# Kernel tuning notes

Measured on AMD Instinct MI355X. Metric: run time of the kernel, lower is better.

## Reference

```python
import jax, jax.numpy as jnp
import numpy as np

B, E, D, H = 4096, 16, 512, 2048

def setup_inputs() -> dict:
    key = jax.random.key(0)
    k1, k2, k3, k4 = jax.random.split(key, 4)
    semantic_vec = jax.random.normal(k1, (B, D), dtype=jnp.float32)
    field_centers = jax.random.normal(k2, (E, D), dtype=jnp.float32)
    # Kaiming-uniform-ish Linear init scale
    lim = 1.0 / np.sqrt(D)
    W = jax.random.uniform(k3, (E, H, D), dtype=jnp.float32, minval=-lim, maxval=lim)
    b = jax.random.uniform(k4, (E, H), dtype=jnp.float32, minval=-lim, maxval=lim)
    return {"semantic_vec": semantic_vec, "field_centers": field_centers, "W": W, "b": b}

def reference(semantic_vec, field_centers, W, b):
    # Each expert e: relu((x - c_e) @ W_e^T + b_e); sum over experts.
    # Use linearity: (x - c_e) @ W_e^T = x @ W_e^T - c_e @ W_e^T, avoiding the [B,E,D] offsets tensor.
    xw = jnp.einsum('bd,ehd->beh', semantic_vec, W)          # [B,E,H]
    cw = jnp.einsum('ed,ehd->eh', field_centers, W)          # [E,H]
    pre = xw - cw[None, :, :] + b[None, :, :]                # [B,E,H]
    feature_anchor = jnp.sum(jax.nn.relu(pre), axis=1)       # [B,H]
    return feature_anchor
```

## Files before the change

### kernel.cpp

```cpp
#include <hip/hip_runtime.h>
#include <hip/hip_bf16.h>
#include <stdint.h>
#include <stddef.h>


#define B_DIM 4096
#define E_DIM 16
#define D_DIM 512
#define H_DIM 2048

typedef short bf16x8 __attribute__((ext_vector_type(8)));
typedef float f32x4 __attribute__((ext_vector_type(4)));

__device__ __forceinline__ short f2bf(float f) {
  __hip_bfloat16 h = __float2bfloat16(f);
  return *reinterpret_cast<short*>(&h);
}

__device__ __forceinline__ bf16x8 cvt8(float4 a, float4 b) {
  bf16x8 v;
  v[0] = f2bf(a.x); v[1] = f2bf(a.y); v[2] = f2bf(a.z); v[3] = f2bf(a.w);
  v[4] = f2bf(b.x); v[5] = f2bf(b.y); v[6] = f2bf(b.z); v[7] = f2bf(b.w);
  return v;
}

__device__ __forceinline__ void async_copy16(const void* gptr, void* lptr) {
  __builtin_amdgcn_global_load_lds(
      (const __attribute__((address_space(1))) void*)gptr,
      (__attribute__((address_space(3))) void*)lptr,
      16, 0, 0);
}

__global__ __launch_bounds__(256) void prep_w(
    const float* __restrict__ W, const float* __restrict__ C,
    const float* __restrict__ bias, __hip_bfloat16* __restrict__ Wb,
    float* __restrict__ bias2) {
  const int gw = (blockIdx.x * 256 + threadIdx.x) >> 6;
  const int lane = threadIdx.x & 63;
  const int e = gw >> 11;

  const float* wr = W + (size_t)gw * D_DIM + lane * 8;
  const float* cr = C + (size_t)e * D_DIM + lane * 8;
  float4 w0 = *(const float4*)(wr);
  float4 w1 = *(const float4*)(wr + 4);
  float4 c0 = *(const float4*)(cr);
  float4 c1 = *(const float4*)(cr + 4);

  *(bf16x8*)((__hip_bfloat16*)Wb + (size_t)gw * D_DIM + lane * 8) = cvt8(w0, w1);

  float dot = w0.x * c0.x + w0.y * c0.y + w0.z * c0.z + w0.w * c0.w +
              w1.x * c1.x + w1.y * c1.y + w1.z * c1.z + w1.w * c1.w;
#pragma unroll
  for (int off = 32; off > 0; off >>= 1) dot += __shfl_down(dot, off, 64);
  if (lane == 0) bias2[gw] = bias[gw] - dot;
}

__global__ __launch_bounds__(256) void conv_x(
    const float* __restrict__ X, __hip_bfloat16* __restrict__ Xb) {
  const size_t i = ((size_t)blockIdx.x * 256 + threadIdx.x) * 8;
  float4 a = *(const float4*)(X + i);
  float4 b = *(const float4*)(X + i + 4);
  *(bf16x8*)(Xb + i) = cvt8(a, b);
}

__global__ __launch_bounds__(256, 2) void moe_gemm(
    const __hip_bfloat16* __restrict__ Xb,
    const __hip_bfloat16* __restrict__ Wb,
    const float* __restrict__ bias2,
    float* __restrict__ out) {
  __shared__ __align__(16) __hip_bfloat16 As[2][128 * 32];
  __shared__ __align__(16) __hip_bfloat16 Bs0[2][128 * 32];
  __shared__ __align__(16) __hip_bfloat16 Bs1[2][128 * 32];
  __shared__ __align__(16) float biasS[E_DIM * 128];

  const int tid = threadIdx.x;
  const int lane = tid & 63;
  const int wave = tid >> 6;
  const int hi = blockIdx.x & 15;
  const int mi = blockIdx.x >> 4;
  const int m0 = mi * 128;
  const int h0 = hi * 128;

  for (int idx = tid; idx < E_DIM * 128; idx += 256) {
    biasS[idx] = bias2[((idx >> 7) << 7 << 4) + h0 + (idx & 127)];
  }

  const int wm = (wave & 1) * 64;
  const int wn = (wave >> 1) * 64;
  const int lm = lane & 15;
  const int q = lane >> 4;

  const int r = tid >> 2;
  const int col = (tid & 3) << 3;
  const size_t aOff0 = (size_t)(m0 + r) * D_DIM + col;
  const size_t aOff1 = (size_t)(m0 + r + 64) * D_DIM + col;
  const size_t bOff0 = (size_t)(h0 + r) * D_DIM + col;
  const size_t bOff1 = (size_t)(h0 + r + 64) * D_DIM + col;
  const int ld0 = tid * 8;
  const int ld1 = (tid + 256) * 8;

  int offA[4], offB[4];
#pragma unroll
  for (int i = 0; i < 4; ++i) offA[i] = (wm + i * 16 + lm) * 32 + q * 8;
#pragma unroll
  for (int j = 0; j < 4; ++j) offB[j] = (wn + j * 16 + lm) * 32 + q * 8;

  f32x4 sum[4][4], acc0[4][4], acc1[4][4];
#pragma unroll
  for (int i = 0; i < 4; ++i)
#pragma unroll
    for (int j = 0; j < 4; ++j) {
      sum[i][j] = (f32x4){0.f, 0.f, 0.f, 0.f};
      acc0[i][j] = (f32x4){0.f, 0.f, 0.f, 0.f};
      acc1[i][j] = (f32x4){0.f, 0.f, 0.f, 0.f};
    }

#define STAGE(buf, tt)                                                       \
  {                                                                          \
    const int kk = ((tt) & 15) << 5;                                         \
    const __hip_bfloat16* Bb = Wb + ((size_t)((tt) >> 4) << 21);             \
    async_copy16(Xb + aOff0 + kk, &As[buf][ld0]);                            \
    async_copy16(Xb + aOff1 + kk, &As[buf][ld1]);                            \
    async_copy16(Bb + bOff0 + kk, &Bs0[buf][ld0]);                           \
    async_copy16(Bb + bOff1 + kk, &Bs0[buf][ld1]);                           \
    async_copy16(Bb + bOff0 + kk + (size_t)H_DIM * D_DIM, &Bs1[buf][ld0]);   \
    async_copy16(Bb + bOff1 + kk + (size_t)H_DIM * D_DIM, &Bs1[buf][ld1]);   \
  }

  STAGE(0, 0);
  __syncthreads();

  for (int t = 0; t < 128; ++t) {
    const int cur = t & 1;
    if (t < 127) STAGE(cur ^ 1, t + 1);

    bf16x8 af[4];
#pragma unroll
    for (int i = 0; i < 4; ++i) af[i] = *(const bf16x8*)&As[cur][offA[i]];
#pragma unroll
    for (int j = 0; j < 4; ++j) {
      const bf16x8 b0 = *(const bf16x8*)&Bs0[cur][offB[j]];
#pragma unroll
      for (int i = 0; i < 4; ++i)
        acc0[i][j] = __builtin_amdgcn_mfma_f32_16x16x32_bf16(
            af[i], b0, acc0[i][j], 0, 0, 0);
      const bf16x8 b1 = *(const bf16x8*)&Bs1[cur][offB[j]];
#pragma unroll
      for (int i = 0; i < 4; ++i)
        acc1[i][j] = __builtin_amdgcn_mfma_f32_16x16x32_bf16(
            af[i], b1, acc1[i][j], 0, 0, 0);
    }

    if ((t & 15) == 15) {
      const int pair = t >> 4;
#pragma unroll
      for (int j = 0; j < 4; ++j) {
        const float bv0 = biasS[(2 * pair) * 128 + wn + j * 16 + lm];
        const float bv1 = biasS[(2 * pair + 1) * 128 + wn + j * 16 + lm];
#pragma unroll
        for (int i = 0; i < 4; ++i)
#pragma unroll
          for (int u = 0; u < 4; ++u) {
            sum[i][j][u] += fmaxf(acc0[i][j][u] + bv0, 0.f) +
                            fmaxf(acc1[i][j][u] + bv1, 0.f);
            acc0[i][j][u] = 0.f;
            acc1[i][j][u] = 0.f;
          }
      }
    }

    __syncthreads();
  }
#undef STAGE

  const int rbase = q * 4;
#pragma unroll
  for (int i = 0; i < 4; ++i)
#pragma unroll
    for (int j = 0; j < 4; ++j)
#pragma unroll
      for (int u = 0; u < 4; ++u)
        out[(size_t)(m0 + wm + i * 16 + rbase + u) * H_DIM + h0 + wn + j * 16 + lm] =
            sum[i][j][u];
}

__global__ __launch_bounds__(256) void naive_kernel(
    const float* __restrict__ x, const float* __restrict__ c,
    const float* __restrict__ W, const float* __restrict__ bias,
    float* __restrict__ out) {
  const int idx = blockIdx.x * 256 + threadIdx.x;
  const int b = idx >> 11;
  const int h = idx & (H_DIM - 1);
  const float* xr = x + (size_t)b * D_DIM;
  float s = 0.f;
  for (int e = 0; e < E_DIM; ++e) {
    const float* wr = W + ((size_t)e * H_DIM + h) * D_DIM;
    const float* cr = c + (size_t)e * D_DIM;
    float acc = bias[e * H_DIM + h];
    for (int d = 0; d < D_DIM; ++d) acc += (xr[d] - cr[d]) * wr[d];
    s += fmaxf(acc, 0.f);
  }
  out[idx] = s;
}

extern "C" void kernel_launch(void* const* d_in, const int* in_sizes, int n_in,
                              void* d_out, int out_size, void* d_ws, size_t ws_size,
                              hipStream_t stream) {
  const float* x = (const float*)d_in[0];
  const float* c = (const float*)d_in[1];
  const float* W = (const float*)d_in[2];
  const float* b = (const float*)d_in[3];
  float* out = (float*)d_out;

  const size_t sz_wb = (size_t)E_DIM * H_DIM * D_DIM * 2;
  const size_t sz_xb = (size_t)B_DIM * D_DIM * 2;
  const size_t sz_b2 = (size_t)E_DIM * H_DIM * 4;
  const size_t need = sz_wb + sz_xb + sz_b2;

  if (ws_size >= need) {
    __hip_bfloat16* Wb = (__hip_bfloat16*)((char*)d_ws);
    __hip_bfloat16* Xb = (__hip_bfloat16*)((char*)d_ws + sz_wb);
    float* bias2 = (float*)((char*)d_ws + sz_wb + sz_xb);
    prep_w<<<8192, 256, 0, stream>>>(W, c, b, Wb, bias2);
    conv_x<<<1024, 256, 0, stream>>>(x, Xb);
    moe_gemm<<<512, 256, 0, stream>>>(Xb, Wb, bias2, out);
  } else {
    naive_kernel<<<(B_DIM * H_DIM) / 256, 256, 0, stream>>>(x, c, W, b, out);
  }
}
```

Measured before the change: 262.3 us.

## Load W operands directly from global into registers, halve N tile, merge prep kernels

The prep and x-conversion kernels are merged into one launch. The GEMM tile shrinks from 128x128 to 128x64 so twice as many blocks run, and occupancy is raised to 4 blocks per CU. W fragments are now read straight from global memory into registers instead of being staged through LDS, which frees shared memory and removes the B staging copies. The cost is uncoalesced, unpipelined global loads of W on the critical path of every k-step, and A tiles in LDS are now reused over fewer output columns.

```diff
diff --git a/kernel.cpp b/kernel.cpp
--- a/kernel.cpp
+++ b/kernel.cpp
@@ -31,62 +31,60 @@
       16, 0, 0);
 }
 
-__global__ __launch_bounds__(256) void prep_w(
+__global__ __launch_bounds__(256) void prep(
     const float* __restrict__ W, const float* __restrict__ C,
-    const float* __restrict__ bias, __hip_bfloat16* __restrict__ Wb,
-    float* __restrict__ bias2) {
-  const int gw = (blockIdx.x * 256 + threadIdx.x) >> 6;
-  const int lane = threadIdx.x & 63;
-  const int e = gw >> 11;
-
-  const float* wr = W + (size_t)gw * D_DIM + lane * 8;
-  const float* cr = C + (size_t)e * D_DIM + lane * 8;
-  float4 w0 = *(const float4*)(wr);
-  float4 w1 = *(const float4*)(wr + 4);
-  float4 c0 = *(const float4*)(cr);
-  float4 c1 = *(const float4*)(cr + 4);
-
-  *(bf16x8*)((__hip_bfloat16*)Wb + (size_t)gw * D_DIM + lane * 8) = cvt8(w0, w1);
-
-  float dot = w0.x * c0.x + w0.y * c0.y + w0.z * c0.z + w0.w * c0.w +
-              w1.x * c1.x + w1.y * c1.y + w1.z * c1.z + w1.w * c1.w;
-#pragma unroll
-  for (int off = 32; off > 0; off >>= 1) dot += __shfl_down(dot, off, 64);
-  if (lane == 0) bias2[gw] = bias[gw] - dot;
-}
-
-__global__ __launch_bounds__(256) void conv_x(
-    const float* __restrict__ X, __hip_bfloat16* __restrict__ Xb) {
-  const size_t i = ((size_t)blockIdx.x * 256 + threadIdx.x) * 8;
-  float4 a = *(const float4*)(X + i);
-  float4 b = *(const float4*)(X + i + 4);
-  *(bf16x8*)(Xb + i) = cvt8(a, b);
-}
-
-__global__ __launch_bounds__(256, 2) void moe_gemm(
+    const float* __restrict__ bias, const float* __restrict__ X,
+    __hip_bfloat16* __restrict__ Wb, float* __restrict__ bias2,
+    __hip_bfloat16* __restrict__ Xb) {
+  if (blockIdx.x < 8192) {
+    const int gw = (blockIdx.x * 256 + threadIdx.x) >> 6;
+    const int lane = threadIdx.x & 63;
+    const int e = gw >> 11;
+
+    const float* wr = W + (size_t)gw * D_DIM + lane * 8;
+    const float* cr = C + (size_t)e * D_DIM + lane * 8;
+    float4 w0 = *(const float4*)(wr);
+    float4 w1 = *(const float4*)(wr + 4);
+    float4 c0 = *(const float4*)(cr);
+    float4 c1 = *(const float4*)(cr + 4);
+
+    *(bf16x8*)(Wb + (size_t)gw * D_DIM + lane * 8) = cvt8(w0, w1);
+
+    float dot = w0.x * c0.x + w0.y * c0.y + w0.z * c0.z + w0.w * c0.w +
+                w1.x * c1.x + w1.y * c1.y + w1.z * c1.z + w1.w * c1.w;
+#pragma unroll
+    for (int off = 32; off > 0; off >>= 1) dot += __shfl_down(dot, off, 64);
+    if (lane == 0) bias2[gw] = bias[gw] - dot;
+  } else {
+    const size_t i = ((size_t)(blockIdx.x - 8192) * 256 + threadIdx.x) * 8;
+    float4 a = *(const float4*)(X + i);
+    float4 b = *(const float4*)(X + i + 4);
+    *(bf16x8*)(Xb + i) = cvt8(a, b);
+  }
+}
+
+__global__ __launch_bounds__(256, 4) void moe_gemm(
     const __hip_bfloat16* __restrict__ Xb,
     const __hip_bfloat16* __restrict__ Wb,
     const float* __restrict__ bias2,
     float* __restrict__ out) {
   __shared__ __align__(16) __hip_bfloat16 As[2][128 * 32];
-  __shared__ __align__(16) __hip_bfloat16 Bs0[2][128 * 32];
-  __shared__ __align__(16) __hip_bfloat16 Bs1[2][128 * 32];
-  __shared__ __align__(16) float biasS[E_DIM * 128];
+  __shared__ __align__(16) float biasS[E_DIM * 64];
 
   const int tid = threadIdx.x;
   const int lane = tid & 63;
   const int wave = tid >> 6;
-  const int hi = blockIdx.x & 15;
-  const int mi = blockIdx.x >> 4;
+  const int hi = blockIdx.x & 31;
+  const int mi = blockIdx.x >> 5;
   const int m0 = mi * 128;
-  const int h0 = hi * 128;
-
-  for (int idx = tid; idx < E_DIM * 128; idx += 256) {
-    biasS[idx] = bias2[((idx >> 7) << 7 << 4) + h0 + (idx & 127)];
+  const int h0 = hi * 64;
+
+  for (int idx = tid; idx < E_DIM * 64; idx += 256) {
+    biasS[idx] = bias2[((idx >> 6) << 11) + h0 + (idx & 63)];
   }
 
   const int wm = (wave & 1) * 64;
-  const int wn = (wave >> 1) * 64;
+  const int wn = (wave >> 1) * 32;
   const int lm = lane & 15;
   const int q = lane >> 4;
 
@@ -94,90 +92,88 @@
   const int col = (tid & 3) << 3;
   const size_t aOff0 = (size_t)(m0 + r) * D_DIM + col;
   const size_t aOff1 = (size_t)(m0 + r + 64) * D_DIM + col;
-  const size_t bOff0 = (size_t)(h0 + r) * D_DIM + col;
-  const size_t bOff1 = (size_t)(h0 + r + 64) * D_DIM + col;
   const int ld0 = tid * 8;
   const int ld1 = (tid + 256) * 8;
 
-  int offA[4], offB[4];
+  int offA[4];
 #pragma unroll
   for (int i = 0; i < 4; ++i) offA[i] = (wm + i * 16 + lm) * 32 + q * 8;
-#pragma unroll
-  for (int j = 0; j < 4; ++j) offB[j] = (wn + j * 16 + lm) * 32 + q * 8;
-
-  f32x4 sum[4][4], acc0[4][4], acc1[4][4];
+
+  const size_t bBase = (size_t)(h0 + wn + lm) * D_DIM + q * 8;
+
+  f32x4 sum[4][2], acc0[4][2], acc1[4][2];
 #pragma unroll
   for (int i = 0; i < 4; ++i)
 #pragma unroll
-    for (int j = 0; j < 4; ++j) {
+    for (int j = 0; j < 2; ++j) {
       sum[i][j] = (f32x4){0.f, 0.f, 0.f, 0.f};
       acc0[i][j] = (f32x4){0.f, 0.f, 0.f, 0.f};
       acc1[i][j] = (f32x4){0.f, 0.f, 0.f, 0.f};
     }
 
-#define STAGE(buf, tt)                                                       \
-  {                                                                          \
-    const int kk = ((tt) & 15) << 5;                                         \
-    const __hip_bfloat16* Bb = Wb + ((size_t)((tt) >> 4) << 21);             \
-    async_copy16(Xb + aOff0 + kk, &As[buf][ld0]);                            \
-    async_copy16(Xb + aOff1 + kk, &As[buf][ld1]);                            \
-    async_copy16(Bb + bOff0 + kk, &Bs0[buf][ld0]);                           \
-    async_copy16(Bb + bOff1 + kk, &Bs0[buf][ld1]);                           \
-    async_copy16(Bb + bOff0 + kk + (size_t)H_DIM * D_DIM, &Bs1[buf][ld0]);   \
-    async_copy16(Bb + bOff1 + kk + (size_t)H_DIM * D_DIM, &Bs1[buf][ld1]);   \
-  }
-
-  STAGE(0, 0);
+#define STAGE_A(buf, kidx)                                        \
+  {                                                               \
+    const int kk = (kidx) << 5;                                   \
+    async_copy16(Xb + aOff0 + kk, &As[buf][ld0]);                 \
+    async_copy16(Xb + aOff1 + kk, &As[buf][ld1]);                 \
+  }
+
+  STAGE_A(0, 0);
   __syncthreads();
 
-  for (int t = 0; t < 128; ++t) {
-    const int cur = t & 1;
-    if (t < 127) STAGE(cur ^ 1, t + 1);
-
-    bf16x8 af[4];
-#pragma unroll
-    for (int i = 0; i < 4; ++i) af[i] = *(const bf16x8*)&As[cur][offA[i]];
-#pragma unroll
-    for (int j = 0; j < 4; ++j) {
-      const bf16x8 b0 = *(const bf16x8*)&Bs0[cur][offB[j]];
+  for (int pair = 0; pair < 8; ++pair) {
+    const __hip_bfloat16* B0 = Wb + ((size_t)(2 * pair) << 20) + bBase;
+    const __hip_bfloat16* B1 = B0 + ((size_t)1 << 20);
+
+#pragma unroll
+    for (int ks = 0; ks < 16; ++ks) {
+      const int t = pair * 16 + ks;
+      const int cur = t & 1;
+      if (t < 127) STAGE_A(cur ^ 1, (t + 1) & 15);
+
+      const int kk = ks << 5;
+      bf16x8 b00 = *(const bf16x8*)(B0 + kk);
+      bf16x8 b01 = *(const bf16x8*)(B0 + kk + 16 * D_DIM);
+      bf16x8 b10 = *(const bf16x8*)(B1 + kk);
+      bf16x8 b11 = *(const bf16x8*)(B1 + kk + 16 * D_DIM);
+
+      bf16x8 af[4];
+#pragma unroll
+      for (int i = 0; i < 4; ++i) af[i] = *(const bf16x8*)&As[cur][offA[i]];
+
+#pragma unroll
+      for (int i = 0; i < 4; ++i) {
+        acc0[i][0] = __builtin_amdgcn_mfma_f32_16x16x32_bf16(af[i], b00, acc0[i][0], 0, 0, 0);
+        acc0[i][1] = __builtin_amdgcn_mfma_f32_16x16x32_bf16(af[i], b01, acc0[i][1], 0, 0, 0);
+        acc1[i][0] = __builtin_amdgcn_mfma_f32_16x16x32_bf16(af[i], b10, acc1[i][0], 0, 0, 0);
+        acc1[i][1] = __builtin_amdgcn_mfma_f32_16x16x32_bf16(af[i], b11, acc1[i][1], 0, 0, 0);
+      }
+
+      __syncthreads();
+    }
+
+#pragma unroll
+    for (int j = 0; j < 2; ++j) {
+      const float bv0 = biasS[(2 * pair) * 64 + wn + j * 16 + lm];
+      const float bv1 = biasS[(2 * pair + 1) * 64 + wn + j * 16 + lm];
 #pragma unroll
       for (int i = 0; i < 4; ++i)
-        acc0[i][j] = __builtin_amdgcn_mfma_f32_16x16x32_bf16(
-            af[i], b0, acc0[i][j], 0, 0, 0);
-      const bf16x8 b1 = *(const bf16x8*)&Bs1[cur][offB[j]];
-#pragma unroll
-      for (int i = 0; i < 4; ++i)
-        acc1[i][j] = __builtin_amdgcn_mfma_f32_16x16x32_bf16(
-            af[i], b1, acc1[i][j], 0, 0, 0);
+#pragma unroll
+        for (int u = 0; u < 4; ++u) {
+          sum[i][j][u] += fmaxf(acc0[i][j][u] + bv0, 0.f) +
+                          fmaxf(acc1[i][j][u] + bv1, 0.f);
+          acc0[i][j][u] = 0.f;
+          acc1[i][j][u] = 0.f;
+        }
     }
-
-    if ((t & 15) == 15) {
-      const int pair = t >> 4;
-#pragma unroll
-      for (int j = 0; j < 4; ++j) {
-        const float bv0 = biasS[(2 * pair) * 128 + wn + j * 16 + lm];
-        const float bv1 = biasS[(2 * pair + 1) * 128 + wn + j * 16 + lm];
-#pragma unroll
-        for (int i = 0; i < 4; ++i)
-#pragma unroll
-          for (int u = 0; u < 4; ++u) {
-            sum[i][j][u] += fmaxf(acc0[i][j][u] + bv0, 0.f) +
-                            fmaxf(acc1[i][j][u] + bv1, 0.f);
-            acc0[i][j][u] = 0.f;
-            acc1[i][j][u] = 0.f;
-          }
-      }
-    }
-
-    __syncthreads();
-  }
-#undef STAGE
+  }
+#undef STAGE_A
 
   const int rbase = q * 4;
 #pragma unroll
   for (int i = 0; i < 4; ++i)
 #pragma unroll
-    for (int j = 0; j < 4; ++j)
+    for (int j = 0; j < 2; ++j)
 #pragma unroll
       for (int u = 0; u < 4; ++u)
         out[(size_t)(m0 + wm + i * 16 + rbase + u) * H_DIM + h0 + wn + j * 16 + lm] =
@@ -221,9 +217,8 @@
     __hip_bfloat16* Wb = (__hip_bfloat16*)((char*)d_ws);
     __hip_bfloat16* Xb = (__hip_bfloat16*)((char*)d_ws + sz_wb);
     float* bias2 = (float*)((char*)d_ws + sz_wb + sz_xb);
-    prep_w<<<8192, 256, 0, stream>>>(W, c, b, Wb, bias2);
-    conv_x<<<1024, 256, 0, stream>>>(x, Xb);
-    moe_gemm<<<512, 256, 0, stream>>>(Xb, Wb, bias2, out);
+    prep<<<9216, 256, 0, stream>>>(W, c, b, x, Wb, bias2, Xb);
+    moe_gemm<<<1024, 256, 0, stream>>>(Xb, Wb, bias2, out);
   } else {
     naive_kernel<<<(B_DIM * H_DIM) / 256, 256, 0, stream>>>(x, c, W, b, out);
   }
```

Result: slower. 505.8 us (+92.9%).
